# Kernel optimization log

Hardware: AMD Instinct MI355X
Metric: run time of the kernel (lower is better)

Reference implementation:

```python
import jax, jax.numpy as jnp
import numpy as np

N_OBJ = 8        # objects per sample -> nc2 = 28 pair-nodes per sample (code caps nc2 < 30)
MAX_REL = 10     # relations per sample (num_rel is uniform so total_rels is static)


def setup_inputs() -> dict:
    key = jax.random.key(0)
    k1, k2, k3, k4, k5 = jax.random.split(key, 5)
    B, D, n = 1024, 512, N_OBJ
    iu, ju = np.triu_indices(n, k=1)                     # (i<j) pair layout, lexicographic
    nc2 = iu.shape[0]                                     # 28
    bcol = np.repeat(np.arange(B), nc2)
    slicing_tensor = jnp.asarray(
        np.stack([bcol, np.tile(iu, B), np.tile(ju, B)], axis=1), dtype=jnp.int32)  # [B*nc2, 3]
    spatial_branch_feature_map = jax.random.normal(k1, (B * nc2, D), dtype=jnp.float32)
    W_self = jax.random.normal(k2, (D, D), dtype=jnp.float32) / np.float32(np.sqrt(D))
    W_nbr = jax.random.normal(k3, (D, D), dtype=jnp.float32) / np.float32(np.sqrt(D))
    b = jnp.zeros((D,), dtype=jnp.float32)
    # object_pairs: distinct indices in [0, n)
    i0 = jax.random.randint(k4, (B, MAX_REL), 0, n)
    off = jax.random.randint(k5, (B, MAX_REL), 1, n)
    i1 = (i0 + off) % n
    object_pairs = jnp.stack([i0, i1], axis=-1).astype(jnp.int32)  # [B, MAX_REL, 2]
    num_rel = jnp.full((B,), MAX_REL, dtype=jnp.int32)
    num_obj = jnp.full((B,), n, dtype=jnp.int32)
    return {"spatial_branch_feature_map": spatial_branch_feature_map, "W_self": W_self,
            "W_nbr": W_nbr, "b": b, "slicing_tensor": slicing_tensor,
            "object_pairs": object_pairs, "num_rel": num_rel, "num_obj": num_obj}


def reference(spatial_branch_feature_map, W_self, W_nbr, b,
              slicing_tensor, object_pairs, num_rel, num_obj):
    x = spatial_branch_feature_map
    N, D = x.shape
    B = num_obj.shape[0]
    nc2 = N // B                                          # pair-nodes per sample
    n = N_OBJ
    # --- fully-connected edge index per sample (incl. self-loops), offset per batch ---
    src_l = jnp.repeat(jnp.arange(nc2, dtype=jnp.int32), nc2)   # row0: t1 outer loop
    dst_l = jnp.tile(jnp.arange(nc2, dtype=jnp.int32), nc2)     # row1: t2 inner loop
    offs = (jnp.arange(B, dtype=jnp.int32) * nc2)[:, None]
    src = (src_l[None, :] + offs).reshape(-1)                   # [B*nc2^2]
    dst = (dst_l[None, :] + offs).reshape(-1)
    # --- GNN layer: sum-aggregate neighbor messages, linear + ReLU ---
    agg = jax.ops.segment_sum(x[src], dst, num_segments=N)      # [N, D]
    h = jax.nn.relu(x @ W_self + agg @ W_nbr + b)               # [N, D]
    # --- key-matching gather (replaces nested python-loop boolean matching) ---
    keys = slicing_tensor[:, 0] * (n * n) + slicing_tensor[:, 1] * n + slicing_tensor[:, 2]
    lut = jnp.zeros((B * n * n,), dtype=jnp.int32).at[keys].set(jnp.arange(N, dtype=jnp.int32))
    pmin = jnp.minimum(object_pairs[..., 0], object_pairs[..., 1])
    pmax = jnp.maximum(object_pairs[..., 0], object_pairs[..., 1])
    bidx = jnp.arange(B, dtype=jnp.int32)[:, None]
    rel_keys = (bidx * (n * n) + pmin * n + pmax).reshape(-1)   # [B*MAX_REL]
    rows = lut[rel_keys]
    return h[rows]                                              # [total_rels, D]
```

## Files before the change

kernel.cpp:

```cpp
#include <hip/hip_runtime.h>
#include <hip/hip_bf16.h>
#include <stdint.h>


typedef __bf16 bf16_t;
typedef __bf16 bf16x8 __attribute__((ext_vector_type(8)));
typedef __bf16 bf16x4 __attribute__((ext_vector_type(4)));
typedef float  f32x4  __attribute__((ext_vector_type(4)));

#define D_DIM 512
#define NC2   28
#define NOBJ  8
#define MAXREL 10
#define B_SAMP 1024
#define OUTROWS (B_SAMP * MAXREL)

__device__ __forceinline__ void gload_lds16(const void* g, void* l) {
  __builtin_amdgcn_global_load_lds(
      (const __attribute__((address_space(1))) unsigned int*)g,
      (__attribute__((address_space(3))) unsigned int*)l, 16, 0, 0);
}

__global__ __launch_bounds__(256) void prep_kernel(
    const float* __restrict__ x, const float* __restrict__ Wself,
    const float* __restrict__ Wnbr, const int* __restrict__ pairs,
    bf16_t* __restrict__ Sbf, bf16_t* __restrict__ Abf,
    bf16_t* __restrict__ Wst, bf16_t* __restrict__ Wnt)
{
  const int blk = blockIdx.x, tid = threadIdx.x;
  if (blk < B_SAMP) {
    __shared__ int rel_row[MAXREL];
    __shared__ float4 oddsum[128];
    if (tid < MAXREL) {
      int p0 = pairs[blk * MAXREL * 2 + tid * 2 + 0];
      int p1 = pairs[blk * MAXREL * 2 + tid * 2 + 1];
      int pmin = min(p0, p1), pmax = max(p0, p1);
      rel_row[tid] = 7 * pmin - (pmin * (pmin - 1)) / 2 + (pmax - pmin - 1);
    }
    __syncthreads();

    const int h = tid >> 7, c = tid & 127;
    const float4* x4 = (const float4*)(x + (size_t)blk * NC2 * D_DIM);
    float4 a = {0.f, 0.f, 0.f, 0.f};
    #pragma unroll
    for (int rp = 0; rp < NC2 / 2; ++rp) {
      float4 v = x4[(rp * 2 + h) * 128 + c];
      a.x += v.x; a.y += v.y; a.z += v.z; a.w += v.w;
    }
    if (h) oddsum[c] = a;
    __syncthreads();
    if (!h) {
      float4 b = oddsum[c];
      bf16x4 o = { (bf16_t)(a.x + b.x), (bf16_t)(a.y + b.y),
                   (bf16_t)(a.z + b.z), (bf16_t)(a.w + b.w) };
      *(bf16x4*)(Sbf + (size_t)blk * D_DIM + c * 4) = o;
    }
    #pragma unroll
    for (int j = h; j < MAXREL; j += 2) {
      float4 v = x4[rel_row[j] * 128 + c];
      bf16x4 o = { (bf16_t)v.x, (bf16_t)v.y, (bf16_t)v.z, (bf16_t)v.w };
      *(bf16x4*)(Abf + (size_t)(blk * MAXREL + j) * D_DIM + c * 4) = o;
    }
  } else {
    __shared__ float tile[32][33];
    const int t = blk - B_SAMP;
    const float* W  = (t & 256) ? Wnbr : Wself;
    bf16_t*     Wt  = (t & 256) ? Wnt  : Wst;
    const int r = t & 255;
    const int k0 = (r & 15) * 32, n0 = (r >> 4) * 32;
    const int tx = tid & 31, ty = tid >> 5;
    #pragma unroll
    for (int i = 0; i < 32; i += 8)
      tile[ty + i][tx] = W[(size_t)(k0 + ty + i) * D_DIM + n0 + tx];
    __syncthreads();
    #pragma unroll
    for (int i = 0; i < 32; i += 8)
      Wt[(size_t)(n0 + ty + i) * D_DIM + k0 + tx] = (bf16_t)tile[tx][ty + i];
  }
}

#define SA_BYTES 6144

#define DS_MFMA(AF, BS, BN) do {                                              \
    _Pragma("unroll")                                                         \
    for (int s_ = 0; s_ < 6; ++s_)                                            \
      AF[s_] = *(const bf16x8*)(aC + (s_ * 16 + lr) * 32 + xorc);             \
    _Pragma("unroll")                                                         \
    for (int s_ = 0; s_ < 5; ++s_)                                            \
      acc[s_] = __builtin_amdgcn_mfma_f32_16x16x32_bf16(AF[s_], BS, acc[s_], 0, 0, 0); \
    acc[5] = __builtin_amdgcn_mfma_f32_16x16x32_bf16(AF[5], BN, acc[5], 0, 0, 0); \
  } while (0)

__global__ __launch_bounds__(256, 5) void fused_gemm_kernel(
    const bf16_t* __restrict__ Abf, const bf16_t* __restrict__ Sbf,
    const bf16_t* __restrict__ Wst, const bf16_t* __restrict__ Wnt,
    const float* __restrict__ bias, float* __restrict__ out)
{
  __shared__ __align__(16) unsigned char pool[2 * SA_BYTES];

  const int tid = threadIdx.x;
  const int w = tid >> 6, l = tid & 63;
  const int kg = l >> 4, lr = l & 15;
  const int n0w = blockIdx.y * 64 + w * 16;
  const int arow0 = blockIdx.x * 80;
  const int srow0 = blockIdx.x * 8;

  f32x4 acc[6] = {};

  auto STAGE = [&](int bsel, int k0) {
    bf16_t* aB = (bf16_t*)(pool + bsel * SA_BYTES);
    #pragma unroll
    for (int r = 0; r < 2; ++r) {
      int slot = r * 4 + w;
      if (slot < 6) {
        int c = slot * 64 + l;
        int row = c >> 2, ch = c & 3;
        int sch = ch ^ ((row >> 1) & 3);
        const bf16_t* g = (row < 80)
            ? Abf + (size_t)(arow0 + row) * D_DIM + k0 + sch * 8
            : Sbf + (size_t)(srow0 + (row & 7)) * D_DIM + k0 + sch * 8;
        gload_lds16(g, aB + (size_t)c * 8);
      }
    }
  };

  const bf16_t* pBs = Wst + (size_t)(n0w + lr) * D_DIM + kg * 8;
  const bf16_t* pBn = Wnt + (size_t)(n0w + lr) * D_DIM + kg * 8;

  bf16x8 bsX, bnX, bsY, bnY, af[6];

  STAGE(0, 0);
  bsX = *(const bf16x8*)(pBs);
  bnX = *(const bf16x8*)(pBn);
  asm volatile("s_waitcnt vmcnt(0)" ::: "memory");
  __builtin_amdgcn_s_barrier();

  const int xorc = (kg ^ ((lr >> 1) & 3)) * 8;
  int cur = 0;
  #pragma unroll
  for (int t = 0; t < 16; t += 2) {
    if (t + 1 < 16) {
      STAGE(cur ^ 1, (t + 1) * 32);
      bsY = *(const bf16x8*)(pBs + (t + 1) * 32);
      bnY = *(const bf16x8*)(pBn + (t + 1) * 32);
      if (w < 2) asm volatile("s_waitcnt vmcnt(4)" ::: "memory");
      else       asm volatile("s_waitcnt vmcnt(3)" ::: "memory");
    } else {
      asm volatile("s_waitcnt vmcnt(0)" ::: "memory");
    }
    __builtin_amdgcn_s_barrier();
    {
      const bf16_t* aC = (const bf16_t*)(pool + cur * SA_BYTES);
      DS_MFMA(af, bsX, bnX);
    }
    __builtin_amdgcn_s_barrier();
    cur ^= 1;

    if (t + 2 < 16) {
      STAGE(cur ^ 1, (t + 2) * 32);
      bsX = *(const bf16x8*)(pBs + (t + 2) * 32);
      bnX = *(const bf16x8*)(pBn + (t + 2) * 32);
      if (w < 2) asm volatile("s_waitcnt vmcnt(4)" ::: "memory");
      else       asm volatile("s_waitcnt vmcnt(3)" ::: "memory");
    } else {
      asm volatile("s_waitcnt vmcnt(0)" ::: "memory");
    }
    __builtin_amdgcn_s_barrier();
    {
      const bf16_t* aC = (const bf16_t*)(pool + cur * SA_BYTES);
      DS_MFMA(af, bsY, bnY);
    }
    __builtin_amdgcn_s_barrier();
    cur ^= 1;
  }

  float* Tex = (float*)pool;
  #pragma unroll
  for (int reg = 0; reg < 4; ++reg)
    Tex[(w * 8 + ((kg * 4 + reg) & 7)) * 20 + lr] = acc[5][reg];
  __syncthreads();

  const float bv = bias[n0w + lr];
  #pragma unroll
  for (int s = 0; s < 5; ++s) {
    #pragma unroll
    for (int reg = 0; reg < 4; ++reg) {
      int rloc = s * 16 + kg * 4 + reg;
      int ls = rloc / MAXREL;
      float v = acc[s][reg] + Tex[(w * 8 + ls) * 20 + lr] + bv;
      out[(size_t)(arow0 + rloc) * D_DIM + n0w + lr] = fmaxf(v, 0.0f);
    }
  }
}

extern "C" void kernel_launch(void* const* d_in, const int* in_sizes, int n_in,
                              void* d_out, int out_size, void* d_ws, size_t ws_size,
                              hipStream_t stream) {
  const float* x     = (const float*)d_in[0];
  const float* Wself = (const float*)d_in[1];
  const float* Wnbr  = (const float*)d_in[2];
  const float* bias  = (const float*)d_in[3];
  const int*   pairs = (const int*)d_in[5];

  char* ws = (char*)d_ws;
  size_t off = 0;
  bf16_t* Sbf = (bf16_t*)(ws + off); off += (size_t)B_SAMP * D_DIM * 2;
  bf16_t* Wst = (bf16_t*)(ws + off); off += (size_t)D_DIM * D_DIM * 2;
  bf16_t* Wnt = (bf16_t*)(ws + off); off += (size_t)D_DIM * D_DIM * 2;
  bf16_t* Abf = (bf16_t*)(ws + off); off += (size_t)OUTROWS * D_DIM * 2;

  prep_kernel<<<B_SAMP + 512, 256, 0, stream>>>(
      x, Wself, Wnbr, pairs, Sbf, Abf, Wst, Wnt);
  fused_gemm_kernel<<<dim3(OUTROWS / 80, D_DIM / 64), 256, 0, stream>>>(
      Abf, Sbf, Wst, Wnt, bias, (float*)d_out);
}
```

Baseline: 40.33 us.

## Pre-swizzle weights into MFMA fragment order and use plain syncthreads pipeline

```diff
diff --git a/kernel.cpp b/kernel.cpp
--- a/kernel.cpp
+++ b/kernel.cpp
@@ -25,7 +25,7 @@
     const float* __restrict__ x, const float* __restrict__ Wself,
     const float* __restrict__ Wnbr, const int* __restrict__ pairs,
     bf16_t* __restrict__ Sbf, bf16_t* __restrict__ Abf,
-    bf16_t* __restrict__ Wst, bf16_t* __restrict__ Wnt)
+    bf16_t* __restrict__ Wsf, bf16_t* __restrict__ Wnf)
 {
   const int blk = blockIdx.x, tid = threadIdx.x;
   if (blk < B_SAMP) {
@@ -62,38 +62,46 @@
       *(bf16x4*)(Abf + (size_t)(blk * MAXREL + j) * D_DIM + c * 4) = o;
     }
   } else {
-    __shared__ float tile[32][33];
-    const int t = blk - B_SAMP;
-    const float* W  = (t & 256) ? Wnbr : Wself;
-    bf16_t*     Wt  = (t & 256) ? Wnt  : Wst;
-    const int r = t & 255;
-    const int k0 = (r & 15) * 32, n0 = (r >> 4) * 32;
+    __shared__ float tile[32 * 33];
+    const int r = blk - B_SAMP;
+    const float* W  = (r & 256) ? Wnbr : Wself;
+    bf16_t*     Wf  = (r & 256) ? Wnf  : Wsf;
+    const int piece = r & 255;
+    const int tstep = piece & 15, nblk = piece >> 4;
+    const int k0 = tstep * 32, n0 = nblk * 32;
     const int tx = tid & 31, ty = tid >> 5;
     #pragma unroll
     for (int i = 0; i < 32; i += 8)
-      tile[ty + i][tx] = W[(size_t)(k0 + ty + i) * D_DIM + n0 + tx];
-    __syncthreads();
-    #pragma unroll
-    for (int i = 0; i < 32; i += 8)
-      Wt[(size_t)(n0 + ty + i) * D_DIM + k0 + tx] = (bf16_t)tile[tx][ty + i];
+      tile[(ty + i) * 33 + tx] = W[(size_t)(k0 + ty + i) * D_DIM + n0 + tx];
+    __syncthreads();
+    const int cfl = tid >> 7, rem = tid & 127;
+    const int ll = rem >> 1, eh = rem & 1;
+    const int kb = (ll >> 4) * 8 + eh * 4;
+    const int nl = cfl * 16 + (ll & 15);
+    bf16x4 o = { (bf16_t)tile[(kb + 0) * 33 + nl], (bf16_t)tile[(kb + 1) * 33 + nl],
+                 (bf16_t)tile[(kb + 2) * 33 + nl], (bf16_t)tile[(kb + 3) * 33 + nl] };
+    const int cf = nblk * 2 + cfl;
+    *(bf16x4*)(Wf + ((size_t)(cf * 16 + tstep) * 64 + ll) * 8 + eh * 4) = o;
   }
 }
 
 #define SA_BYTES 6144
 
-#define DS_MFMA(AF, BS, BN) do {                                              \
+#define DO_STEP(BS, BN) do {                                                  \
+    const bf16_t* aC = (const bf16_t*)(pool + cur * SA_BYTES);                \
+    bf16x8 af[6];                                                             \
     _Pragma("unroll")                                                         \
     for (int s_ = 0; s_ < 6; ++s_)                                            \
-      AF[s_] = *(const bf16x8*)(aC + (s_ * 16 + lr) * 32 + xorc);             \
+      af[s_] = *(const bf16x8*)(aC + (s_ * 16 + lr) * 32 + xorc);             \
     _Pragma("unroll")                                                         \
     for (int s_ = 0; s_ < 5; ++s_)                                            \
-      acc[s_] = __builtin_amdgcn_mfma_f32_16x16x32_bf16(AF[s_], BS, acc[s_], 0, 0, 0); \
-    acc[5] = __builtin_amdgcn_mfma_f32_16x16x32_bf16(AF[5], BN, acc[5], 0, 0, 0); \
+      acc[s_] = __builtin_amdgcn_mfma_f32_16x16x32_bf16(af[s_], BS, acc[s_], 0, 0, 0); \
+    acc[5] = __builtin_amdgcn_mfma_f32_16x16x32_bf16(af[5], BN, acc[5], 0, 0, 0); \
   } while (0)
 
 __global__ __launch_bounds__(256, 5) void fused_gemm_kernel(
     const bf16_t* __restrict__ Abf, const bf16_t* __restrict__ Sbf,
-    const bf16_t* __restrict__ Wst, const bf16_t* __restrict__ Wnt,
+    const bf16_t* __restrict__ Wsf, const bf16_t* __restrict__ Wnf,
     const float* __restrict__ bias, float* __restrict__ out)
 {
   __shared__ __align__(16) unsigned char pool[2 * SA_BYTES];
@@ -104,6 +112,10 @@
   const int n0w = blockIdx.y * 64 + w * 16;
   const int arow0 = blockIdx.x * 80;
   const int srow0 = blockIdx.x * 8;
+  const int cf = blockIdx.y * 4 + w;
+
+  const bf16_t* pBs = Wsf + (size_t)cf * 16 * 512 + (size_t)l * 8;
+  const bf16_t* pBn = Wnf + (size_t)cf * 16 * 512 + (size_t)l * 8;
 
   f32x4 acc[6] = {};
 
@@ -124,16 +136,11 @@
     }
   };
 
-  const bf16_t* pBs = Wst + (size_t)(n0w + lr) * D_DIM + kg * 8;
-  const bf16_t* pBn = Wnt + (size_t)(n0w + lr) * D_DIM + kg * 8;
-
-  bf16x8 bsX, bnX, bsY, bnY, af[6];
-
+  bf16x8 bsX, bnX, bsY, bnY;
   STAGE(0, 0);
   bsX = *(const bf16x8*)(pBs);
   bnX = *(const bf16x8*)(pBn);
-  asm volatile("s_waitcnt vmcnt(0)" ::: "memory");
-  __builtin_amdgcn_s_barrier();
+  __syncthreads();
 
   const int xorc = (kg ^ ((lr >> 1) & 3)) * 8;
   int cur = 0;
@@ -141,36 +148,20 @@
   for (int t = 0; t < 16; t += 2) {
     if (t + 1 < 16) {
       STAGE(cur ^ 1, (t + 1) * 32);
-      bsY = *(const bf16x8*)(pBs + (t + 1) * 32);
-      bnY = *(const bf16x8*)(pBn + (t + 1) * 32);
-      if (w < 2) asm volatile("s_waitcnt vmcnt(4)" ::: "memory");
-      else       asm volatile("s_waitcnt vmcnt(3)" ::: "memory");
-    } else {
-      asm volatile("s_waitcnt vmcnt(0)" ::: "memory");
-    }
-    __builtin_amdgcn_s_barrier();
-    {
-      const bf16_t* aC = (const bf16_t*)(pool + cur * SA_BYTES);
-      DS_MFMA(af, bsX, bnX);
-    }
-    __builtin_amdgcn_s_barrier();
+      bsY = *(const bf16x8*)(pBs + (t + 1) * 512);
+      bnY = *(const bf16x8*)(pBn + (t + 1) * 512);
+    }
+    DO_STEP(bsX, bnX);
+    __syncthreads();
     cur ^= 1;
 
     if (t + 2 < 16) {
       STAGE(cur ^ 1, (t + 2) * 32);
-      bsX = *(const bf16x8*)(pBs + (t + 2) * 32);
-      bnX = *(const bf16x8*)(pBn + (t + 2) * 32);
-      if (w < 2) asm volatile("s_waitcnt vmcnt(4)" ::: "memory");
-      else       asm volatile("s_waitcnt vmcnt(3)" ::: "memory");
-    } else {
-      asm volatile("s_waitcnt vmcnt(0)" ::: "memory");
-    }
-    __builtin_amdgcn_s_barrier();
-    {
-      const bf16_t* aC = (const bf16_t*)(pool + cur * SA_BYTES);
-      DS_MFMA(af, bsY, bnY);
-    }
-    __builtin_amdgcn_s_barrier();
+      bsX = *(const bf16x8*)(pBs + (t + 2) * 512);
+      bnX = *(const bf16x8*)(pBn + (t + 2) * 512);
+    }
+    DO_STEP(bsY, bnY);
+    __syncthreads();
     cur ^= 1;
   }
 
@@ -205,12 +196,12 @@
   char* ws = (char*)d_ws;
   size_t off = 0;
   bf16_t* Sbf = (bf16_t*)(ws + off); off += (size_t)B_SAMP * D_DIM * 2;
-  bf16_t* Wst = (bf16_t*)(ws + off); off += (size_t)D_DIM * D_DIM * 2;
-  bf16_t* Wnt = (bf16_t*)(ws + off); off += (size_t)D_DIM * D_DIM * 2;
+  bf16_t* Wsf = (bf16_t*)(ws + off); off += (size_t)D_DIM * D_DIM * 2;
+  bf16_t* Wnf = (bf16_t*)(ws + off); off += (size_t)D_DIM * D_DIM * 2;
   bf16_t* Abf = (bf16_t*)(ws + off); off += (size_t)OUTROWS * D_DIM * 2;
 
   prep_kernel<<<B_SAMP + 512, 256, 0, stream>>>(
-      x, Wself, Wnbr, pairs, Sbf, Abf, Wst, Wnt);
+      x, Wself, Wnbr, pairs, Sbf, Abf, Wsf, Wnf);
   fused_gemm_kernel<<<dim3(OUTROWS / 80, D_DIM / 64), 256, 0, stream>>>(
-      Abf, Sbf, Wst, Wnt, bias, (float*)d_out);
-}
+      Abf, Sbf, Wsf, Wnf, bias, (float*)d_out);
+}
```

Result: faster. 32.71 us, median of 2 (-18.9%).
